# Kernel tuning notes

Measured on AMD Instinct MI355X. Metric: run time of the kernel, lower is better.

The kernel has to match this reference:

```python
import jax, jax.numpy as jnp
import numpy as np

N_NODES = 100000
N_FEAT = 512
HIDDEN = 16
N_CLASSES = 7
N_EDGES = 3200000


def gcn_conv(x, W, b, src, dst, num_nodes):
    """GCNConv: add self-loops, symmetric deg^-1/2 normalization, linear, aggregate."""
    loop = jnp.arange(num_nodes, dtype=src.dtype)
    src2 = jnp.concatenate([src, loop])  # [E+N]
    dst2 = jnp.concatenate([dst, loop])
    ones = jnp.ones(src2.shape[0], dtype=x.dtype)
    deg = jax.ops.segment_sum(ones, dst2, num_segments=num_nodes)  # in-degree incl. self-loop
    dinv = jnp.where(deg > 0, jax.lax.rsqrt(deg), 0.0)
    norm = dinv[src2] * dinv[dst2]  # [E+N]
    h = x @ W  # [N, out] -- transform before gather (small out dim)
    msg = h[src2] * norm[:, None]  # gather + scale
    out = jax.ops.segment_sum(msg, dst2, num_segments=num_nodes)  # scatter-add
    return out + b


def setup_inputs() -> dict:
    key = jax.random.key(0)
    k1, k2, k3, k4, k5 = jax.random.split(key, 5)
    x = jax.random.normal(k1, (N_NODES, N_FEAT), dtype=jnp.float32)
    edge_index = jax.random.randint(k2, (2, N_EDGES), 0, N_NODES, dtype=jnp.int64)
    # Glorot init like PyG GCNConv
    W1 = jax.random.normal(k3, (N_FEAT, HIDDEN), dtype=jnp.float32) * np.sqrt(2.0 / (N_FEAT + HIDDEN))
    b1 = jnp.zeros((HIDDEN,), dtype=jnp.float32)
    W2 = jax.random.normal(k4, (HIDDEN, N_CLASSES), dtype=jnp.float32) * np.sqrt(2.0 / (HIDDEN + N_CLASSES))
    b2 = jnp.zeros((N_CLASSES,), dtype=jnp.float32)
    return {"x": x, "edge_index": edge_index, "W1": W1, "b1": b1, "W2": W2, "b2": b2}


def reference(x, edge_index, W1, b1, W2, b2):
    src, dst = edge_index[0], edge_index[1]
    h = gcn_conv(x, W1, b1, src, dst, N_NODES)
    h = jax.nn.relu(h)
    # F.dropout(training=self.training): identity in eval mode (deterministic reference)
    h = gcn_conv(h, W2, b2, src, dst, N_NODES)
    return jax.nn.log_softmax(h, axis=1)
```

## Files before the change

### kernel.cpp

```cpp
#include <hip/hip_runtime.h>
#include <math.h>

#define N_NODES   100000
#define N_FEAT    512
#define HIDDEN    16
#define N_CLASSES 7
#define N_EDGES   3200000

#define BSHIFT 7
#define BNODES 128
#define BMASK  127
#define NBUK   782
#define CHUNK  16384
#define NCHUNK 196
#define CAP    6144

typedef short v8s __attribute__((ext_vector_type(8)));
typedef float v4f __attribute__((ext_vector_type(4)));

__device__ __forceinline__ float bf_lo(unsigned int p) { return __uint_as_float(p << 16); }
__device__ __forceinline__ float bf_hi(unsigned int p) { return __uint_as_float(p & 0xffff0000u); }
__device__ __forceinline__ unsigned int pack_bf2(float a, float b) {
    unsigned int ua = __float_as_uint(a); ua += 0x7fffu + ((ua >> 16) & 1u);
    unsigned int ub = __float_as_uint(b); ub += 0x7fffu + ((ub >> 16) & 1u);
    return (ua >> 16) | (ub & 0xffff0000u);
}


__global__ __launch_bounds__(256) void k_hist(const int* __restrict__ dst,
                                              int* __restrict__ hglob) {
    __shared__ int h[NBUK];
    int tid = threadIdx.x;
    for (int i = tid; i < NBUK; i += 256) h[i] = 0;
    __syncthreads();
    int base = blockIdx.x * CHUNK;
    for (int i = tid; i < CHUNK; i += 256) {
        int e = base + i;
        if (e < N_EDGES) atomicAdd(&h[dst[e] >> BSHIFT], 1);
    }
    __syncthreads();
    for (int i = tid; i < NBUK; i += 256)
        hglob[blockIdx.x * NBUK + i] = h[i];
}


__global__ __launch_bounds__(1024) void k_scan(const int* __restrict__ hglob,
                                               int* __restrict__ btot,
                                               int* __restrict__ gbase,
                                               int* __restrict__ hpre) {
    __shared__ int sd[1024];
    int t = threadIdx.x;
    int tot = 0;
    if (t < NBUK)
        for (int c = 0; c < NCHUNK; c++) tot += hglob[c * NBUK + t];
    sd[t] = (t < NBUK) ? tot : 0;
    __syncthreads();
    for (int off = 1; off < 1024; off <<= 1) {
        int a = (t >= off) ? sd[t - off] : 0;
        __syncthreads();
        sd[t] += a;
        __syncthreads();
    }
    if (t < NBUK) {
        int ex = sd[t] - tot;
        btot[t] = tot;
        gbase[t] = ex;
        int run = ex;
        for (int c = 0; c < NCHUNK; c++) {
            hpre[c * NBUK + t] = run;
            run += hglob[c * NBUK + t];
        }
    }
}


__global__ __launch_bounds__(256) void k_scatter(const int* __restrict__ src,
                                                 const int* __restrict__ dst,
                                                 const int* __restrict__ hpre,
                                                 int* __restrict__ entries) {
    __shared__ int lb[NBUK];
    __shared__ int cur[NBUK];
    int tid = threadIdx.x;
    for (int i = tid; i < NBUK; i += 256) {
        lb[i] = hpre[blockIdx.x * NBUK + i];
        cur[i] = 0;
    }
    __syncthreads();
    int base = blockIdx.x * CHUNK;
    for (int i = tid; i < CHUNK; i += 256) {
        int e = base + i;
        if (e < N_EDGES) {
            int d = dst[e];
            int b = d >> BSHIFT;
            int pos = lb[b] + atomicAdd(&cur[b], 1);
            entries[pos] = src[e] | ((d & BMASK) << 17);
        }
    }
}


__global__ __launch_bounds__(512) void k_nodesort(int* __restrict__ entries,
                                                  const int* __restrict__ btot,
                                                  const int* __restrict__ gbase,
                                                  float* __restrict__ dinv,
                                                  int* __restrict__ nodeptr) {
    __shared__ int ebuf[CAP];
    __shared__ int hcnt[BNODES];
    __shared__ int hincl[BNODES];
    __shared__ int hcur[BNODES];
    int tid = threadIdx.x;
    int bk = blockIdx.x;
    int cnt = btot[bk], base = gbase[bk];
    if (cnt > CAP) cnt = CAP;
    if (tid < BNODES) hcnt[tid] = 0;
    __syncthreads();
    for (int i = tid; i < cnt; i += 512) {
        int en = entries[base + i];
        ebuf[i] = en;
        atomicAdd(&hcnt[en >> 17], 1);
    }
    __syncthreads();
    if (tid < BNODES) hincl[tid] = hcnt[tid];
    __syncthreads();
    for (int off = 1; off < BNODES; off <<= 1) {
        int v = 0;
        if (tid < BNODES && tid >= off) v = hincl[tid - off];
        __syncthreads();
        if (tid < BNODES) hincl[tid] += v;
        __syncthreads();
    }
    if (tid < BNODES) {
        int excl = hincl[tid] - hcnt[tid];
        hcur[tid] = excl;
        int n = bk * BNODES + tid;
        if (n < N_NODES) {
            nodeptr[n] = base + excl;
            dinv[n]    = rsqrtf((float)(hcnt[tid] + 1));
        } else if (n == N_NODES) {
            nodeptr[n] = base + excl;
        }
    }
    __syncthreads();
    for (int i = tid; i < cnt; i += 512) {
        int en = ebuf[i];
        int pos = atomicAdd(&hcur[en >> 17], 1);
        entries[base + pos] = en & 0x1FFFF;
    }
}


__global__ __launch_bounds__(256) void k_gemm1(const float* __restrict__ x,
                                               const float* __restrict__ W1,
                                               const float* __restrict__ dinv,
                                               unsigned int* __restrict__ hs1b) {
    __shared__ unsigned int wfrag[16 * 64 * 4];
    __shared__ unsigned int atile[64 * 68];

    int tid = threadIdx.x;
    int wave = tid >> 6, lane = tid & 63;
    int row0 = blockIdx.x * 64;
    int m = lane & 15, quad = lane >> 4;

    {
        int q0 = tid * 4;
#pragma unroll
        for (int qq = 0; qq < 4; qq++) {
            int q = q0 + qq;
            int s = q >> 6, l = q & 63;
            int n = l & 15, kb = s * 32 + (l >> 4) * 8;
            unsigned int* wp = &wfrag[q * 4];
#pragma unroll
            for (int h = 0; h < 4; h++)
                wp[h] = pack_bf2(W1[(kb + 2 * h) * 16 + n],
                                 W1[(kb + 2 * h + 1) * 16 + n]);
        }
    }

    v4f acc = {0.f, 0.f, 0.f, 0.f};

    for (int c = 0; c < 4; c++) {
        __syncthreads();
#pragma unroll
        for (int i = 0; i < 8; i++) {
            int f = i * 256 + tid;
            int r = f >> 5, c4 = f & 31;
            int grow = row0 + r;
            float4 xv = make_float4(0.f, 0.f, 0.f, 0.f);
            if (grow < N_NODES)
                xv = *(const float4*)(x + (size_t)grow * N_FEAT + c * 128 + c4 * 4);
            unsigned int* ap = &atile[r * 68 + c4 * 2];
            ap[0] = pack_bf2(xv.x, xv.y);
            ap[1] = pack_bf2(xv.z, xv.w);
        }
        __syncthreads();
#pragma unroll
        for (int s = 0; s < 4; s++) {
            v8s af = *(const v8s*)&atile[(wave * 16 + m) * 68 + s * 16 + quad * 4];
            v8s bf = *(const v8s*)&wfrag[((c * 4 + s) * 64 + lane) * 4];
            acc = __builtin_amdgcn_mfma_f32_16x16x32_bf16(af, bf, acc, 0, 0, 0);
        }
    }

    __syncthreads();
    float* dt = (float*)atile;
    {
        float* wdt = dt + wave * 272;
        int col = lane & 15;
#pragma unroll
        for (int r = 0; r < 4; r++)
            wdt[(quad * 4 + r) * 17 + col] = acc[r];
    }
    __syncthreads();
    {
        int row = tid >> 2, p = tid & 3;
        int grow = row0 + row;
        if (grow < N_NODES) {
            float dn = dinv[grow];
            float* wdt = dt + (row >> 4) * 272 + (row & 15) * 17 + 4 * p;
            unsigned int d0 = pack_bf2(dn * wdt[0], dn * wdt[1]);
            unsigned int d1 = pack_bf2(dn * wdt[2], dn * wdt[3]);
            *(uint2*)(hs1b + (size_t)grow * 8 + 2 * p) = make_uint2(d0, d1);
        }
    }
}


__global__ __launch_bounds__(512) void k_agg1(const unsigned int* __restrict__ hs1b,
                                              const int* __restrict__ srt,
                                              const int* __restrict__ nodeptr,
                                              const float* __restrict__ dinv,
                                              const float* __restrict__ b1,
                                              const float* __restrict__ W2,
                                              unsigned int* __restrict__ hs2b) {
    __shared__ float w2l[HIDDEN * N_CLASSES];
    __shared__ float b1l[HIDDEN];
    int tid = threadIdx.x;
    if (tid < HIDDEN * N_CLASSES) w2l[tid] = W2[tid];
    if (tid < HIDDEN) b1l[tid] = b1[tid];
    __syncthreads();

    int bk = blockIdx.x;
    int g = tid >> 3, j = tid & 7;

#pragma unroll
    for (int rep = 0; rep < 2; rep++) {
        int l = g + rep * 64;
        int n = bk * BNODES + l;
        float t[7] = {0.f, 0.f, 0.f, 0.f, 0.f, 0.f, 0.f};
        float dn = 0.f;
        if (n < N_NODES) {
            int p0 = nodeptr[n], p1 = nodeptr[n + 1];
            float aL0 = 0, aH0 = 0, aL1 = 0, aH1 = 0;
            float aL2 = 0, aH2 = 0, aL3 = 0, aH3 = 0;
            int e = p0;
            for (; e + 4 <= p1; e += 4) {
                int s0 = srt[e], s1 = srt[e + 1], s2 = srt[e + 2], s3 = srt[e + 3];
                unsigned int v0 = hs1b[(size_t)s0 * 8 + j];
                unsigned int v1 = hs1b[(size_t)s1 * 8 + j];
                unsigned int v2 = hs1b[(size_t)s2 * 8 + j];
                unsigned int v3 = hs1b[(size_t)s3 * 8 + j];
                aL0 += bf_lo(v0); aH0 += bf_hi(v0);
                aL1 += bf_lo(v1); aH1 += bf_hi(v1);
                aL2 += bf_lo(v2); aH2 += bf_hi(v2);
                aL3 += bf_lo(v3); aH3 += bf_hi(v3);
            }
            for (; e < p1; e++) {
                unsigned int v = hs1b[(size_t)srt[e] * 8 + j];
                aL0 += bf_lo(v); aH0 += bf_hi(v);
            }
            unsigned int sv = hs1b[(size_t)n * 8 + j];
            float accL = aL0 + aL1 + aL2 + aL3 + bf_lo(sv);
            float accH = aH0 + aH1 + aH2 + aH3 + bf_hi(sv);
            dn = dinv[n];
            float z0 = fmaxf(dn * accL + b1l[2 * j],     0.f);
            float z1 = fmaxf(dn * accH + b1l[2 * j + 1], 0.f);
            const float* wr0 = &w2l[(2 * j) * 7];
            const float* wr1 = &w2l[(2 * j + 1) * 7];
#pragma unroll
            for (int q = 0; q < 7; q++) t[q] = z0 * wr0[q] + z1 * wr1[q];
        }
#pragma unroll
        for (int mk = 1; mk < 8; mk <<= 1) {
#pragma unroll
            for (int q = 0; q < 7; q++) t[q] += __shfl_xor(t[q], mk, 64);
        }
        if (j == 0 && n < N_NODES) {
            uint4* o = (uint4*)(hs2b + (size_t)n * 4);
            o[0] = make_uint4(pack_bf2(dn * t[0], dn * t[1]),
                              pack_bf2(dn * t[2], dn * t[3]),
                              pack_bf2(dn * t[4], dn * t[5]),
                              pack_bf2(dn * t[6], 0.f));
        }
    }
}


__global__ __launch_bounds__(512) void k_agg2(const unsigned int* __restrict__ hs2b,
                                              const int* __restrict__ srt,
                                              const int* __restrict__ nodeptr,
                                              const float* __restrict__ dinv,
                                              const float* __restrict__ b2,
                                              float* __restrict__ out) {
    int tid = threadIdx.x;
    int g = tid >> 2, j = tid & 3;
    int bk = blockIdx.x;
    int n = bk * BNODES + g;
    bool valid = (n < N_NODES);
    float lL = -3.4e38f, lH = -3.4e38f;
    if (valid) {
        int p0 = nodeptr[n], p1 = nodeptr[n + 1];
        float aL0 = 0, aH0 = 0, aL1 = 0, aH1 = 0;
        float aL2 = 0, aH2 = 0, aL3 = 0, aH3 = 0;
        int e = p0;
        for (; e + 4 <= p1; e += 4) {
            int s0 = srt[e], s1 = srt[e + 1], s2 = srt[e + 2], s3 = srt[e + 3];
            unsigned int v0 = hs2b[(size_t)s0 * 4 + j];
            unsigned int v1 = hs2b[(size_t)s1 * 4 + j];
            unsigned int v2 = hs2b[(size_t)s2 * 4 + j];
            unsigned int v3 = hs2b[(size_t)s3 * 4 + j];
            aL0 += bf_lo(v0); aH0 += bf_hi(v0);
            aL1 += bf_lo(v1); aH1 += bf_hi(v1);
            aL2 += bf_lo(v2); aH2 += bf_hi(v2);
            aL3 += bf_lo(v3); aH3 += bf_hi(v3);
        }
        for (; e < p1; e++) {
            unsigned int v = hs2b[(size_t)srt[e] * 4 + j];
            aL0 += bf_lo(v); aH0 += bf_hi(v);
        }
        unsigned int sv = hs2b[(size_t)n * 4 + j];
        float accL = aL0 + aL1 + aL2 + aL3 + bf_lo(sv);
        float accH = aH0 + aH1 + aH2 + aH3 + bf_hi(sv);
        float dn = dinv[n];
        lL = dn * accL + b2[2 * j];
        int cch = 2 * j + 1;
        lH = (cch < 7) ? (dn * accH + b2[cch]) : -3.4e38f;
    }
    float mm = fmaxf(lL, lH);
    mm = fmaxf(mm, __shfl_xor(mm, 1, 64));
    mm = fmaxf(mm, __shfl_xor(mm, 2, 64));
    float s = 0.f;
    if (valid) {
        s = expf(lL - mm);
        if (2 * j + 1 < 7) s += expf(lH - mm);
    }
    s += __shfl_xor(s, 1, 64);
    s += __shfl_xor(s, 2, 64);
    if (valid) {
        float ls = mm + logf(s);
        out[(size_t)n * 7 + 2 * j] = lL - ls;
        if (2 * j + 1 < 7) out[(size_t)n * 7 + 2 * j + 1] = lH - ls;
    }
}


extern "C" void kernel_launch(void* const* d_in, const int* in_sizes, int n_in,
                              void* d_out, int out_size, void* d_ws, size_t ws_size,
                              hipStream_t stream) {
    const float* x  = (const float*)d_in[0];
    const int*   ei = (const int*)d_in[1];
    const float* W1 = (const float*)d_in[2];
    const float* b1 = (const float*)d_in[3];
    const float* W2 = (const float*)d_in[4];
    const float* b2 = (const float*)d_in[5];
    float* out = (float*)d_out;

    const int* src = ei;
    const int* dst = ei + N_EDGES;

    char* w = (char*)d_ws;
    int*          btot    = (int*)(w + 0);
    int*          gbase   = (int*)(w + 4096);
    float*        dinv    = (float*)(w + 8192);
    int*          nodeptr = (int*)(w + 408576);
    int*          hglob   = (int*)(w + 808960);
    int*          hpre    = (int*)(w + 1422336);
    unsigned int* hs1b    = (unsigned int*)(w + 2036736);
    unsigned int* hs2b    = (unsigned int*)(w + 5236736);
    int*          entries = (int*)(w + 6836736);

    k_hist    <<<NCHUNK, 256, 0, stream>>>(dst, hglob);
    k_scan    <<<1, 1024, 0, stream>>>(hglob, btot, gbase, hpre);
    k_scatter <<<NCHUNK, 256, 0, stream>>>(src, dst, hpre, entries);
    k_nodesort<<<NBUK, 512, 0, stream>>>(entries, btot, gbase, dinv, nodeptr);
    k_gemm1   <<<1563, 256, 0, stream>>>(x, W1, dinv, hs1b);
    k_agg1    <<<NBUK, 512, 0, stream>>>(hs1b, entries, nodeptr, dinv, b1, W2, hs2b);
    k_agg2    <<<NBUK, 512, 0, stream>>>(hs2b, entries, nodeptr, dinv, b2, out);
}
```

Measured before the change: 512.9 us.

## Vectorize aggregation gathers to uint4 and split edges across lanes; widen hist/scatter blocks

In the first aggregation, each node now uses 2 lanes that each load 16-byte uint4 rows instead of 8 lanes loading 4-byte words. The node's edge list is split in half across two thread groups, and the partial sums are combined through shared memory. The second aggregation gives each lane a quarter of the edge range and loads the full 8-bf16 row as one uint4, then reduces with shuffles before a single-lane log-softmax. The histogram and scatter kernels now run with 1024 threads per block. The goal is fewer, wider memory transactions in the latency-bound gathers, at the cost of an extra barrier, shared-memory traffic and serial softmax work.

```diff
diff --git a/kernel.cpp b/kernel.cpp
--- a/kernel.cpp
+++ b/kernel.cpp
@@ -27,19 +27,19 @@
 }
 
 
-__global__ __launch_bounds__(256) void k_hist(const int* __restrict__ dst,
-                                              int* __restrict__ hglob) {
+__global__ __launch_bounds__(1024) void k_hist(const int* __restrict__ dst,
+                                               int* __restrict__ hglob) {
     __shared__ int h[NBUK];
     int tid = threadIdx.x;
-    for (int i = tid; i < NBUK; i += 256) h[i] = 0;
+    for (int i = tid; i < NBUK; i += 1024) h[i] = 0;
     __syncthreads();
     int base = blockIdx.x * CHUNK;
-    for (int i = tid; i < CHUNK; i += 256) {
+    for (int i = tid; i < CHUNK; i += 1024) {
         int e = base + i;
         if (e < N_EDGES) atomicAdd(&h[dst[e] >> BSHIFT], 1);
     }
     __syncthreads();
-    for (int i = tid; i < NBUK; i += 256)
+    for (int i = tid; i < NBUK; i += 1024)
         hglob[blockIdx.x * NBUK + i] = h[i];
 }
 
@@ -74,20 +74,20 @@
 }
 
 
-__global__ __launch_bounds__(256) void k_scatter(const int* __restrict__ src,
-                                                 const int* __restrict__ dst,
-                                                 const int* __restrict__ hpre,
-                                                 int* __restrict__ entries) {
+__global__ __launch_bounds__(1024) void k_scatter(const int* __restrict__ src,
+                                                  const int* __restrict__ dst,
+                                                  const int* __restrict__ hpre,
+                                                  int* __restrict__ entries) {
     __shared__ int lb[NBUK];
     __shared__ int cur[NBUK];
     int tid = threadIdx.x;
-    for (int i = tid; i < NBUK; i += 256) {
+    for (int i = tid; i < NBUK; i += 1024) {
         lb[i] = hpre[blockIdx.x * NBUK + i];
         cur[i] = 0;
     }
     __syncthreads();
     int base = blockIdx.x * CHUNK;
-    for (int i = tid; i < CHUNK; i += 256) {
+    for (int i = tid; i < CHUNK; i += 1024) {
         int e = base + i;
         if (e < N_EDGES) {
             int d = dst[e];
@@ -234,62 +234,90 @@
                                               unsigned int* __restrict__ hs2b) {
     __shared__ float w2l[HIDDEN * N_CLASSES];
     __shared__ float b1l[HIDDEN];
+    __shared__ float part[BNODES][17];
     int tid = threadIdx.x;
     if (tid < HIDDEN * N_CLASSES) w2l[tid] = W2[tid];
     if (tid < HIDDEN) b1l[tid] = b1[tid];
-    __syncthreads();
 
     int bk = blockIdx.x;
-    int g = tid >> 3, j = tid & 7;
-
-#pragma unroll
-    for (int rep = 0; rep < 2; rep++) {
-        int l = g + rep * 64;
-        int n = bk * BNODES + l;
+    int g = tid >> 1, j = tid & 1;
+    int l = g & (BNODES - 1), half = g >> 7;
+    int n = bk * BNODES + l;
+    bool valid = (n < N_NODES);
+
+    float accL[4] = {0.f, 0.f, 0.f, 0.f};
+    float accH[4] = {0.f, 0.f, 0.f, 0.f};
+    const uint4* hv = (const uint4*)hs1b;
+
+    if (valid) {
+        int p0 = nodeptr[n], p1 = nodeptr[n + 1];
+        int mid = p0 + ((p1 - p0) >> 1);
+        int e0 = half ? mid : p0;
+        int e1 = half ? p1 : mid;
+        int e = e0;
+        for (; e + 4 <= e1; e += 4) {
+            int s[4];
+            uint4 v[4];
+#pragma unroll
+            for (int u = 0; u < 4; u++) s[u] = srt[e + u];
+#pragma unroll
+            for (int u = 0; u < 4; u++) v[u] = hv[(size_t)s[u] * 2 + j];
+#pragma unroll
+            for (int u = 0; u < 4; u++) {
+                accL[0] += bf_lo(v[u].x); accH[0] += bf_hi(v[u].x);
+                accL[1] += bf_lo(v[u].y); accH[1] += bf_hi(v[u].y);
+                accL[2] += bf_lo(v[u].z); accH[2] += bf_hi(v[u].z);
+                accL[3] += bf_lo(v[u].w); accH[3] += bf_hi(v[u].w);
+            }
+        }
+        for (; e < e1; e++) {
+            uint4 v0 = hv[(size_t)srt[e] * 2 + j];
+            accL[0] += bf_lo(v0.x); accH[0] += bf_hi(v0.x);
+            accL[1] += bf_lo(v0.y); accH[1] += bf_hi(v0.y);
+            accL[2] += bf_lo(v0.z); accH[2] += bf_hi(v0.z);
+            accL[3] += bf_lo(v0.w); accH[3] += bf_hi(v0.w);
+        }
+        if (half == 0) {
+            uint4 sv = hv[(size_t)n * 2 + j];
+            accL[0] += bf_lo(sv.x); accH[0] += bf_hi(sv.x);
+            accL[1] += bf_lo(sv.y); accH[1] += bf_hi(sv.y);
+            accL[2] += bf_lo(sv.z); accH[2] += bf_hi(sv.z);
+            accL[3] += bf_lo(sv.w); accH[3] += bf_hi(sv.w);
+        }
+    }
+
+    if (half == 1 && valid) {
+#pragma unroll
+        for (int q = 0; q < 4; q++) {
+            int ch = j * 8 + 2 * q;
+            part[l][ch]     = accL[q];
+            part[l][ch + 1] = accH[q];
+        }
+    }
+    __syncthreads();
+
+    if (half == 0 && valid) {
+        float dn = dinv[n];
         float t[7] = {0.f, 0.f, 0.f, 0.f, 0.f, 0.f, 0.f};
-        float dn = 0.f;
-        if (n < N_NODES) {
-            int p0 = nodeptr[n], p1 = nodeptr[n + 1];
-            float aL0 = 0, aH0 = 0, aL1 = 0, aH1 = 0;
-            float aL2 = 0, aH2 = 0, aL3 = 0, aH3 = 0;
-            int e = p0;
-            for (; e + 4 <= p1; e += 4) {
-                int s0 = srt[e], s1 = srt[e + 1], s2 = srt[e + 2], s3 = srt[e + 3];
-                unsigned int v0 = hs1b[(size_t)s0 * 8 + j];
-                unsigned int v1 = hs1b[(size_t)s1 * 8 + j];
-                unsigned int v2 = hs1b[(size_t)s2 * 8 + j];
-                unsigned int v3 = hs1b[(size_t)s3 * 8 + j];
-                aL0 += bf_lo(v0); aH0 += bf_hi(v0);
-                aL1 += bf_lo(v1); aH1 += bf_hi(v1);
-                aL2 += bf_lo(v2); aH2 += bf_hi(v2);
-                aL3 += bf_lo(v3); aH3 += bf_hi(v3);
-            }
-            for (; e < p1; e++) {
-                unsigned int v = hs1b[(size_t)srt[e] * 8 + j];
-                aL0 += bf_lo(v); aH0 += bf_hi(v);
-            }
-            unsigned int sv = hs1b[(size_t)n * 8 + j];
-            float accL = aL0 + aL1 + aL2 + aL3 + bf_lo(sv);
-            float accH = aH0 + aH1 + aH2 + aH3 + bf_hi(sv);
-            dn = dinv[n];
-            float z0 = fmaxf(dn * accL + b1l[2 * j],     0.f);
-            float z1 = fmaxf(dn * accH + b1l[2 * j + 1], 0.f);
-            const float* wr0 = &w2l[(2 * j) * 7];
-            const float* wr1 = &w2l[(2 * j + 1) * 7];
-#pragma unroll
-            for (int q = 0; q < 7; q++) t[q] = z0 * wr0[q] + z1 * wr1[q];
-        }
-#pragma unroll
-        for (int mk = 1; mk < 8; mk <<= 1) {
-#pragma unroll
-            for (int q = 0; q < 7; q++) t[q] += __shfl_xor(t[q], mk, 64);
-        }
-        if (j == 0 && n < N_NODES) {
-            uint4* o = (uint4*)(hs2b + (size_t)n * 4);
-            o[0] = make_uint4(pack_bf2(dn * t[0], dn * t[1]),
-                              pack_bf2(dn * t[2], dn * t[3]),
-                              pack_bf2(dn * t[4], dn * t[5]),
-                              pack_bf2(dn * t[6], 0.f));
+#pragma unroll
+        for (int q = 0; q < 4; q++) {
+            int ch = j * 8 + 2 * q;
+            float z0 = fmaxf(dn * (accL[q] + part[l][ch])     + b1l[ch],     0.f);
+            float z1 = fmaxf(dn * (accH[q] + part[l][ch + 1]) + b1l[ch + 1], 0.f);
+            const float* w0 = &w2l[ch * 7];
+            const float* w1 = &w2l[(ch + 1) * 7];
+#pragma unroll
+            for (int k = 0; k < 7; k++) t[k] += z0 * w0[k] + z1 * w1[k];
+        }
+#pragma unroll
+        for (int k = 0; k < 7; k++) t[k] += __shfl_xor(t[k], 1, 64);
+        if (j == 0) {
+            uint4 o;
+            o.x = pack_bf2(dn * t[0], dn * t[1]);
+            o.y = pack_bf2(dn * t[2], dn * t[3]);
+            o.z = pack_bf2(dn * t[4], dn * t[5]);
+            o.w = pack_bf2(dn * t[6], 0.f);
+            ((uint4*)hs2b)[n] = o;
         }
     }
 }
@@ -302,53 +330,69 @@
                                               const float* __restrict__ b2,
                                               float* __restrict__ out) {
     int tid = threadIdx.x;
-    int g = tid >> 2, j = tid & 3;
     int bk = blockIdx.x;
-    int n = bk * BNODES + g;
+    int l = tid >> 2, h = tid & 3;
+    int n = bk * BNODES + l;
     bool valid = (n < N_NODES);
-    float lL = -3.4e38f, lH = -3.4e38f;
+
+    float a[8] = {0.f, 0.f, 0.f, 0.f, 0.f, 0.f, 0.f, 0.f};
+    const uint4* hv = (const uint4*)hs2b;
+
     if (valid) {
         int p0 = nodeptr[n], p1 = nodeptr[n + 1];
-        float aL0 = 0, aH0 = 0, aL1 = 0, aH1 = 0;
-        float aL2 = 0, aH2 = 0, aL3 = 0, aH3 = 0;
-        int e = p0;
-        for (; e + 4 <= p1; e += 4) {
-            int s0 = srt[e], s1 = srt[e + 1], s2 = srt[e + 2], s3 = srt[e + 3];
-            unsigned int v0 = hs2b[(size_t)s0 * 4 + j];
-            unsigned int v1 = hs2b[(size_t)s1 * 4 + j];
-            unsigned int v2 = hs2b[(size_t)s2 * 4 + j];
-            unsigned int v3 = hs2b[(size_t)s3 * 4 + j];
-            aL0 += bf_lo(v0); aH0 += bf_hi(v0);
-            aL1 += bf_lo(v1); aH1 += bf_hi(v1);
-            aL2 += bf_lo(v2); aH2 += bf_hi(v2);
-            aL3 += bf_lo(v3); aH3 += bf_hi(v3);
-        }
-        for (; e < p1; e++) {
-            unsigned int v = hs2b[(size_t)srt[e] * 4 + j];
-            aL0 += bf_lo(v); aH0 += bf_hi(v);
-        }
-        unsigned int sv = hs2b[(size_t)n * 4 + j];
-        float accL = aL0 + aL1 + aL2 + aL3 + bf_lo(sv);
-        float accH = aH0 + aH1 + aH2 + aH3 + bf_hi(sv);
-        float dn = dinv[n];
-        lL = dn * accL + b2[2 * j];
-        int cch = 2 * j + 1;
-        lH = (cch < 7) ? (dn * accH + b2[cch]) : -3.4e38f;
-    }
-    float mm = fmaxf(lL, lH);
-    mm = fmaxf(mm, __shfl_xor(mm, 1, 64));
-    mm = fmaxf(mm, __shfl_xor(mm, 2, 64));
-    float s = 0.f;
-    if (valid) {
-        s = expf(lL - mm);
-        if (2 * j + 1 < 7) s += expf(lH - mm);
-    }
-    s += __shfl_xor(s, 1, 64);
-    s += __shfl_xor(s, 2, 64);
-    if (valid) {
-        float ls = mm + logf(s);
-        out[(size_t)n * 7 + 2 * j] = lL - ls;
-        if (2 * j + 1 < 7) out[(size_t)n * 7 + 2 * j + 1] = lH - ls;
+        int deg = p1 - p0;
+        int e0 = p0 + ((deg * h) >> 2);
+        int e1 = p0 + ((deg * (h + 1)) >> 2);
+        int e = e0;
+        for (; e + 4 <= e1; e += 4) {
+            int s[4];
+            uint4 v[4];
+#pragma unroll
+            for (int u = 0; u < 4; u++) s[u] = srt[e + u];
+#pragma unroll
+            for (int u = 0; u < 4; u++) v[u] = hv[s[u]];
+#pragma unroll
+            for (int u = 0; u < 4; u++) {
+                a[0] += bf_lo(v[u].x); a[1] += bf_hi(v[u].x);
+                a[2] += bf_lo(v[u].y); a[3] += bf_hi(v[u].y);
+                a[4] += bf_lo(v[u].z); a[5] += bf_hi(v[u].z);
+                a[6] += bf_lo(v[u].w);
+            }
+        }
+        for (; e < e1; e++) {
+            uint4 v0 = hv[srt[e]];
+            a[0] += bf_lo(v0.x); a[1] += bf_hi(v0.x);
+            a[2] += bf_lo(v0.y); a[3] += bf_hi(v0.y);
+            a[4] += bf_lo(v0.z); a[5] += bf_hi(v0.z);
+            a[6] += bf_lo(v0.w);
+        }
+        if (h == 0) {
+            uint4 sv = hv[n];
+            a[0] += bf_lo(sv.x); a[1] += bf_hi(sv.x);
+            a[2] += bf_lo(sv.y); a[3] += bf_hi(sv.y);
+            a[4] += bf_lo(sv.z); a[5] += bf_hi(sv.z);
+            a[6] += bf_lo(sv.w);
+        }
+#pragma unroll
+        for (int q = 0; q < 7; q++) {
+            a[q] += __shfl_xor(a[q], 1, 64);
+            a[q] += __shfl_xor(a[q], 2, 64);
+        }
+        if (h == 0) {
+            float dn = dinv[n];
+            float lg[7];
+#pragma unroll
+            for (int c = 0; c < 7; c++) lg[c] = dn * a[c] + b2[c];
+            float m = lg[0];
+#pragma unroll
+            for (int c = 1; c < 7; c++) m = fmaxf(m, lg[c]);
+            float s = 0.f;
+#pragma unroll
+            for (int c = 0; c < 7; c++) s += expf(lg[c] - m);
+            float ls = m + logf(s);
+#pragma unroll
+            for (int c = 0; c < 7; c++) out[(size_t)n * 7 + c] = lg[c] - ls;
+        }
     }
 }
 
@@ -378,9 +422,9 @@
     unsigned int* hs2b    = (unsigned int*)(w + 5236736);
     int*          entries = (int*)(w + 6836736);
 
-    k_hist    <<<NCHUNK, 256, 0, stream>>>(dst, hglob);
+    k_hist    <<<NCHUNK, 1024, 0, stream>>>(dst, hglob);
     k_scan    <<<1, 1024, 0, stream>>>(hglob, btot, gbase, hpre);
-    k_scatter <<<NCHUNK, 256, 0, stream>>>(src, dst, hpre, entries);
+    k_scatter <<<NCHUNK, 1024, 0, stream>>>(src, dst, hpre, entries);
     k_nodesort<<<NBUK, 512, 0, stream>>>(entries, btot, gbase, dinv, nodeptr);
     k_gemm1   <<<1563, 256, 0, stream>>>(x, W1, dinv, hs1b);
     k_agg1    <<<NBUK, 512, 0, stream>>>(hs1b, entries, nodeptr, dinv, b1, W2, hs2b);
```

Measured after the change: 456.9 us. 10.9% less time.
